# Performance work log

Measured on AMD Instinct MI355X. Metric: run time of the kernel, lower is better.

## Reference

```python
import jax, jax.numpy as jnp
import numpy as np

K = 20          # neighbors per point
EPS = 1e-5      # BatchNorm eps
SLOPE = 0.2     # LeakyReLU negative slope


def _knn(x, k):
    # x: [B, C, N] -> idx [B, N, k] of nearest neighbors in feature space
    sq = jnp.sum(x * x, axis=1)                       # [B, N]
    inner = jnp.einsum('bcn,bcm->bnm', x, x)          # [B, N, N]
    neg_dist = 2.0 * inner - sq[:, :, None] - sq[:, None, :]
    _, idx = jax.lax.top_k(neg_dist, k)
    return idx


def _edge_features(x, idx):
    # x: [B, C, N], idx: [B, N, k] -> edge features [B, 2C, N, k] = cat(x_i, x_j - x_i)
    xt = jnp.transpose(x, (0, 2, 1))                  # [B, N, C]
    nb = jax.vmap(lambda f, i: f[i])(xt, idx)         # [B, N, k, C]
    center = jnp.broadcast_to(xt[:, :, None, :], nb.shape)
    ef = jnp.concatenate([center, nb - center], axis=-1)  # [B, N, k, 2C]
    return jnp.transpose(ef, (0, 3, 1, 2))            # [B, 2C, N, k]


def _bn(t, g, b, axes):
    # BatchNorm (training-mode batch stats), channel axis = 1
    m = jnp.mean(t, axis=axes, keepdims=True)
    v = jnp.var(t, axis=axes, keepdims=True)
    tn = (t - m) * jax.lax.rsqrt(v + EPS)
    shp = [1] * t.ndim
    shp[1] = -1
    return tn * g.reshape(shp) + b.reshape(shp)


def _lrelu(t):
    return jnp.where(t >= 0, t, SLOPE * t)


def _layer2d(t, w, g, b):
    # 1x1 Conv2d (no bias) + BN2d + LeakyReLU over edge tensor [B, C, N, k]
    t = jnp.einsum('bcnk,oc->bonk', t, w)
    return _lrelu(_bn(t, g, b, (0, 2, 3)))


def _multi_edge_conv(x, w1, g1, b1, w2, g2, b2):
    idx = _knn(x, K)
    t = _edge_features(x, idx)
    t = _layer2d(t, w1, g1, b1)
    t = _layer2d(t, w2, g2, b2)
    return jnp.max(t, axis=-1)                        # max over neighbors -> [B, O, N]


def _edge_conv(x, w, g, b):
    idx = _knn(x, K)
    t = _edge_features(x, idx)
    t = _layer2d(t, w, g, b)
    return jnp.max(t, axis=-1)


def _tail(x, w, g, b):
    # 1x1 Conv1d (no bias) + BN1d + LeakyReLU, x: [B, 256, N] -> [B, 128, N]
    t = jnp.einsum('bcn,oc->bon', x, w)
    return _lrelu(_bn(t, g, b, (0, 2)))


def setup_inputs() -> dict:
    key = jax.random.key(0)
    ks = jax.random.split(key, 16)
    B, C, N = 8, 6, 2048

    def w(k, o, i):
        return jax.random.normal(k, (o, i), jnp.float32) * np.sqrt(2.0 / i).astype(np.float32)

    d = {
        'x': jax.random.normal(ks[0], (B, C, N), jnp.float32),
        # MultiEdgeConvolution 0: edge dim 2*6=12 -> 64 -> 64
        'w0a': w(ks[1], 64, 12), 'g0a': jnp.ones(64), 'b0a': jnp.zeros(64),
        'w0b': w(ks[2], 64, 64), 'g0b': jnp.ones(64), 'b0b': jnp.zeros(64),
        # MultiEdgeConvolution 1: edge dim 2*64=128 -> 64 -> 64
        'w1a': w(ks[3], 64, 128), 'g1a': jnp.ones(64), 'b1a': jnp.zeros(64),
        'w1b': w(ks[4], 64, 64), 'g1b': jnp.ones(64), 'b1b': jnp.zeros(64),
        # EdgeConvolution 2 and 3: 128 -> 64
        'w2': w(ks[5], 64, 128), 'g2': jnp.ones(64), 'b2': jnp.zeros(64),
        'w3': w(ks[6], 64, 128), 'g3': jnp.ones(64), 'b3': jnp.zeros(64),
        # Tail: 256 -> 128
        'wt': w(ks[7], 128, 256), 'gt': jnp.ones(128), 'bt': jnp.zeros(128),
    }
    return d


def reference(x, w0a, g0a, b0a, w0b, g0b, b0b,
              w1a, g1a, b1a, w1b, g1b, b1b,
              w2, g2, b2, w3, g3, b3, wt, gt, bt):
    x1 = _multi_edge_conv(x,  w0a, g0a, b0a, w0b, g0b, b0b)   # [B, 64, N]
    x2 = _multi_edge_conv(x1, w1a, g1a, b1a, w1b, g1b, b1b)   # [B, 64, N]
    x3 = _edge_conv(x2, w2, g2, b2)                           # [B, 64, N]
    x4 = _edge_conv(x3, w3, g3, b3)                           # [B, 64, N]
    feats = jnp.concatenate([x1, x2, x3, x4], axis=1)         # [B, 256, N]
    return _tail(feats, wt, gt, bt)                           # [B, 128, N]
```

## Files before the change

### kernel.cpp

```cpp
#include <hip/hip_runtime.h>

constexpr int BB = 8, NN = 2048, KK = 20;
constexpr float SLP = 0.2f;
constexpr float NEG = -3.0e38f;
constexpr float EMPTYV = -3.3e38f;
constexpr double EPSD = 1e-5;

typedef short short8 __attribute__((ext_vector_type(8)));
typedef float f32x4 __attribute__((ext_vector_type(4)));
typedef unsigned short ushort;

__device__ __forceinline__ float lrelu(float v) { return v >= 0.f ? v : SLP * v; }

__device__ __forceinline__ float bits2f(unsigned u) { union { unsigned u; float f; } a; a.u = u; return a.f; }
__device__ __forceinline__ unsigned f2bits(float f) { union { float f; unsigned u; } a; a.f = f; return a.u; }

__device__ __forceinline__ ushort bf16rne(float f) {
  unsigned u = f2bits(f);
  return (ushort)((u + 0x7fffu + ((u >> 16) & 1u)) >> 16);
}

__device__ __forceinline__ void split3(float x, ushort& h, ushort& m, ushort& l) {
  h = bf16rne(x);
  float fh = bits2f(((unsigned)h) << 16);
  float t1 = x - fh;
  m = bf16rne(t1);
  float fm = bits2f(((unsigned)m) << 16);
  float t2 = t1 - fm;
  l = bf16rne(t2);
}

__global__ __launch_bounds__(256) void k_prep0(const float* __restrict__ x, float* __restrict__ x0nc,
                                               ushort* __restrict__ xh, ushort* __restrict__ xm,
                                               ushort* __restrict__ xlo, float* __restrict__ sqb) {
  int i = blockIdx.x * 256 + threadIdx.x;
  if (i >= BB * NN) return;
  int b = i >> 11, n = i & (NN - 1);
  float v[6];
#pragma unroll
  for (int c = 0; c < 6; ++c) v[c] = x[((size_t)b * 6 + c) * NN + n];
  float s = 0.f;
#pragma unroll
  for (int c = 0; c < 6; ++c) s = __fadd_rn(s, __fmul_rn(v[c], v[c]));
  sqb[i] = s;
#pragma unroll
  for (int c = 0; c < 6; ++c) x0nc[(size_t)i * 6 + c] = v[c];
  size_t base = (size_t)i * 32;
#pragma unroll
  for (int c = 0; c < 32; ++c) {
    float xv = (c < 6) ? v[c] : 0.f;
    ushort h, m, l;
    split3(xv, h, m, l);
    xh[base + c] = h; xm[base + c] = m; xlo[base + c] = l;
  }
}

__global__ __launch_bounds__(256) void k_applyprep(float* __restrict__ xio, const double* __restrict__ st,
                                                   const float* __restrict__ g, const float* __restrict__ bb,
                                                   ushort* __restrict__ xh, ushort* __restrict__ xm,
                                                   ushort* __restrict__ xlo, float* __restrict__ sqb) {
  __shared__ float sa[64], sd[64];
  const int tid = threadIdx.x;
  if (tid < 64) {
    constexpr double invM = 1.0 / (double)(BB * NN * KK);
    double sm = st[tid] * invM;
    double ad = (double)g[tid] / sqrt(st[64 + tid] * invM - sm * sm + EPSD);
    sa[tid] = (float)ad;
    sd[tid] = (float)((double)bb[tid] - sm * ad);
  }
  __syncthreads();
  int i = blockIdx.x * 256 + tid;
  float* src = xio + (size_t)i * 64;
  float v[64];
#pragma unroll
  for (int c4 = 0; c4 < 16; ++c4) {
    float4 t = *reinterpret_cast<const float4*>(src + 4 * c4);
    v[4 * c4 + 0] = t.x; v[4 * c4 + 1] = t.y; v[4 * c4 + 2] = t.z; v[4 * c4 + 3] = t.w;
  }
#pragma unroll
  for (int c = 0; c < 64; ++c) v[c] = lrelu(fmaf(sa[c], v[c], sd[c]));
  float s = 0.f;
#pragma unroll
  for (int c = 0; c < 64; ++c) s = __fadd_rn(s, __fmul_rn(v[c], v[c]));
  sqb[i] = s;
#pragma unroll
  for (int c4 = 0; c4 < 16; ++c4) {
    float4 t;
    t.x = v[4 * c4 + 0]; t.y = v[4 * c4 + 1]; t.z = v[4 * c4 + 2]; t.w = v[4 * c4 + 3];
    *reinterpret_cast<float4*>(src + 4 * c4) = t;
  }
  size_t base = (size_t)i * 64;
#pragma unroll
  for (int c = 0; c < 64; ++c) {
    ushort h, m, l;
    split3(v[c], h, m, l);
    xh[base + c] = h; xm[base + c] = m; xlo[base + c] = l;
  }
}

template <int CP>
__global__ __launch_bounds__(256) void k_gram(const ushort* __restrict__ xh, const ushort* __restrict__ xm,
                                              const ushort* __restrict__ xlo, const float* __restrict__ sqb,
                                              float* __restrict__ S, int b0) {
  constexpr int KS = CP / 32;
  const int bl = blockIdx.z, b = b0 + bl;
  const int r0 = blockIdx.x * 32;
  const int cc0 = blockIdx.y * 32;
  const int tid = threadIdx.x, w = tid >> 6, l = tid & 63;
  const int rt = w & 1;
  const size_t xb = (size_t)b * NN * CP;
  const int ko = (l >> 4) * 8;

  short8 Ah[KS], Am[KS], Al[KS];
  const int ar = r0 + rt * 16 + (l & 15);
#pragma unroll
  for (int ks = 0; ks < KS; ++ks) {
    size_t o = xb + (size_t)ar * CP + ks * 32 + ko;
    Ah[ks] = *reinterpret_cast<const short8*>(xh + o);
    Am[ks] = *reinterpret_cast<const short8*>(xm + o);
    Al[ks] = *reinterpret_cast<const short8*>(xlo + o);
  }
  float sqi[4];
  const int rr = r0 + rt * 16 + (l >> 4) * 4;
#pragma unroll
  for (int q = 0; q < 4; ++q) sqi[q] = sqb[b * NN + rr + q];
  const size_t Sbase = ((size_t)bl * NN + rr) * NN;

  int ct = cc0 + (w >> 1);
  short8 Bh[KS], Bm[KS], Bl[KS], Ch[KS], Cm[KS], Cl[KS];
#pragma unroll
  for (int ks = 0; ks < KS; ++ks) {
    size_t o = xb + (size_t)(ct * 16 + (l & 15)) * CP + ks * 32 + ko;
    Bh[ks] = *reinterpret_cast<const short8*>(xh + o);
    Bm[ks] = *reinterpret_cast<const short8*>(xm + o);
    Bl[ks] = *reinterpret_cast<const short8*>(xlo + o);
  }
  for (int t = 0; t < 16; ++t) {
    int nct = ct + 2;
    if (t < 15) {
#pragma unroll
      for (int ks = 0; ks < KS; ++ks) {
        size_t o = xb + (size_t)(nct * 16 + (l & 15)) * CP + ks * 32 + ko;
        Ch[ks] = *reinterpret_cast<const short8*>(xh + o);
        Cm[ks] = *reinterpret_cast<const short8*>(xm + o);
        Cl[ks] = *reinterpret_cast<const short8*>(xlo + o);
      }
    }
    f32x4 acc = {0.f, 0.f, 0.f, 0.f};
#pragma unroll
    for (int ks = 0; ks < KS; ++ks) {
      acc = __builtin_amdgcn_mfma_f32_16x16x32_bf16(Am[ks], Bm[ks], acc, 0, 0, 0);
      acc = __builtin_amdgcn_mfma_f32_16x16x32_bf16(Ah[ks], Bl[ks], acc, 0, 0, 0);
      acc = __builtin_amdgcn_mfma_f32_16x16x32_bf16(Al[ks], Bh[ks], acc, 0, 0, 0);
      acc = __builtin_amdgcn_mfma_f32_16x16x32_bf16(Ah[ks], Bm[ks], acc, 0, 0, 0);
      acc = __builtin_amdgcn_mfma_f32_16x16x32_bf16(Am[ks], Bh[ks], acc, 0, 0, 0);
      acc = __builtin_amdgcn_mfma_f32_16x16x32_bf16(Ah[ks], Bh[ks], acc, 0, 0, 0);
    }
    int col = ct * 16 + (l & 15);
    float sqj = sqb[b * NN + col];
#pragma unroll
    for (int q = 0; q < 4; ++q) {
      float sc = __fsub_rn(__fsub_rn(2.f * acc[q], sqi[q]), sqj);
      S[Sbase + (size_t)q * NN + col] = sc;
    }
#pragma unroll
    for (int ks = 0; ks < KS; ++ks) { Bh[ks] = Ch[ks]; Bm[ks] = Cm[ks]; Bl[ks] = Cl[ks]; }
    ct = nct;
  }
}

__global__ __launch_bounds__(256) void k_select(const float* __restrict__ S, int* __restrict__ idxo, int b0) {
  const int bl = blockIdx.y, b = b0 + bl;
  const int wv = threadIdx.x >> 6, l = threadIdx.x & 63;
  const int row = blockIdx.x * 4 + wv;
  __shared__ float sr[4][2048];
  __shared__ int oid[4][20];
  char* base = reinterpret_cast<char*>(&sr[wv][0]);
  const float* Sp = S + ((size_t)bl * NN + row) * NN;
#pragma unroll
  for (int e = 0; e < 8; ++e) {
    float4 v = *reinterpret_cast<const float4*>(Sp + e * 256 + l * 4);
    int c = e * 64 + l;
    c ^= (c >> 3) & 7;
    *reinterpret_cast<float4*>(base + (c << 4)) = v;
  }
  float v0 = EMPTYV, v1 = EMPTYV;
  int i0 = -1, i1 = -1;
#pragma unroll
  for (int e = 0; e < 8; ++e) {
    int c = l * 8 + e;
    c ^= (c >> 3) & 7;
    float4 v = *reinterpret_cast<const float4*>(base + (c << 4));
    int jb = l * 32 + e * 4;
    float va[4] = {v.x, v.y, v.z, v.w};
#pragma unroll
    for (int q = 0; q < 4; ++q) {
      float vv = va[q];
      int jj = jb + q;
      if (vv > v0) { v1 = v0; i1 = i0; v0 = vv; i0 = jj; }
      else if (vv > v1) { v1 = vv; i1 = jj; }
    }
  }
  for (int e = 0; e < KK; ++e) {
    float m = v0;
#pragma unroll
    for (int d = 1; d < 64; d <<= 1) m = fmaxf(m, __shfl_xor(m, d));
    unsigned long long msk = __ballot(v0 == m);
    int wl = __ffsll((unsigned long long)msk) - 1;
    if (l == wl) {
      oid[wv][e] = i0;
      int j = i0;
      int cc = j >> 2;
      int cs = cc ^ ((cc >> 3) & 7);
      *reinterpret_cast<float*>(base + (cs << 4) + ((j & 3) << 2)) = NEG;
      v0 = v1; i0 = i1; v1 = EMPTYV; i1 = -1;
      if (v0 <= EMPTYV) {
        v0 = EMPTYV; v1 = EMPTYV; i0 = -1; i1 = -1;
#pragma unroll
        for (int e2 = 0; e2 < 8; ++e2) {
          int c = l * 8 + e2;
          c ^= (c >> 3) & 7;
          float4 v = *reinterpret_cast<const float4*>(base + (c << 4));
          int jb = l * 32 + e2 * 4;
          float va[4] = {v.x, v.y, v.z, v.w};
#pragma unroll
          for (int q = 0; q < 4; ++q) {
            float vv = va[q];
            int jj = jb + q;
            if (vv > v0) { v1 = v0; i1 = i0; v0 = vv; i0 = jj; }
            else if (vv > v1) { v1 = vv; i1 = jj; }
          }
        }
      }
    }
  }
  if (l < KK) idxo[((size_t)b * NN + row) * KK + l] = oid[wv][l];
}

template <int C>
__global__ __launch_bounds__(256) void k_uv(const float* __restrict__ xin, const float* __restrict__ w,
                                            float* __restrict__ u, float* __restrict__ v) {
  const int b = blockIdx.y, n0 = blockIdx.x * 4;
  const int tid = threadIdx.x, o = tid & 63, nn = tid >> 6;
  __shared__ float wl[64][2 * C + 1];
  __shared__ float xl[4][C];
  for (int t = tid; t < 64 * 2 * C; t += 256) wl[t / (2 * C)][t % (2 * C)] = w[t];
  for (int t = tid; t < 4 * C; t += 256) xl[t / C][t % C] = xin[((size_t)b * NN + n0 + t / C) * C + t % C];
  __syncthreads();
  float s1 = 0.f, s2 = 0.f;
#pragma unroll
  for (int c = 0; c < C; ++c) {
    float xv = xl[nn][c];
    s1 = fmaf(wl[o][c], xv, s1);
    s2 = fmaf(wl[o][C + c], xv, s2);
  }
  size_t i = ((size_t)b * NN + n0 + nn) * 64 + o;
  u[i] = s1 - s2;
  v[i] = s2;
}

__global__ __launch_bounds__(256) void k_passA(const float* __restrict__ u, const float* __restrict__ v,
                                               const int* __restrict__ idx, double* __restrict__ st) {
  const int b = blockIdx.y, n0 = blockIdx.x * 16;
  const int tid = threadIdx.x, c = tid & 63, nw = tid >> 6;
  double s = 0.0, ss = 0.0;
  for (int nn = nw; nn < 16; nn += 4) {
    size_t nb = (size_t)b * NN + n0 + nn;
    float uu = u[nb * 64 + c];
    const int* ip = idx + nb * KK;
#pragma unroll
    for (int k = 0; k < KK; ++k) {
      float val = uu + v[((size_t)b * NN + ip[k]) * 64 + c];
      double dv = (double)val;
      s += dv; ss = fma(dv, dv, ss);
    }
  }
  __shared__ double red[2][4][64];
  red[0][nw][c] = s; red[1][nw][c] = ss;
  __syncthreads();
  if (tid < 64) {
    double S = red[0][0][tid] + red[0][1][tid] + red[0][2][tid] + red[0][3][tid];
    double SS = red[1][0][tid] + red[1][1][tid] + red[1][2][tid] + red[1][3][tid];
    atomicAdd(&st[tid], S);
    atomicAdd(&st[64 + tid], SS);
  }
}

__global__ __launch_bounds__(256) void k_passAmax(const float* __restrict__ u, const float* __restrict__ v,
                                                  const int* __restrict__ idx, float* __restrict__ xout,
                                                  double* __restrict__ st) {
  const int b = blockIdx.y, n0 = blockIdx.x * 16;
  const int tid = threadIdx.x, c = tid & 63, nw = tid >> 6;
  double s = 0.0, ss = 0.0;
  for (int nn = nw; nn < 16; nn += 4) {
    size_t nb = (size_t)b * NN + n0 + nn;
    float uu = u[nb * 64 + c];
    const int* ip = idx + nb * KK;
    float mx = NEG;
#pragma unroll
    for (int k = 0; k < KK; ++k) {
      float val = uu + v[((size_t)b * NN + ip[k]) * 64 + c];
      mx = fmaxf(mx, val);
      double dv = (double)val;
      s += dv; ss = fma(dv, dv, ss);
    }
    xout[nb * 64 + c] = mx;
  }
  __shared__ double red[2][4][64];
  red[0][nw][c] = s; red[1][nw][c] = ss;
  __syncthreads();
  if (tid < 64) {
    double S = red[0][0][tid] + red[0][1][tid] + red[0][2][tid] + red[0][3][tid];
    double SS = red[1][0][tid] + red[1][1][tid] + red[1][2][tid] + red[1][3][tid];
    atomicAdd(&st[tid], S);
    atomicAdd(&st[64 + tid], SS);
  }
}

__global__ __launch_bounds__(256) void k_passB(const float* __restrict__ u, const float* __restrict__ v,
                                               const int* __restrict__ idx, const double* __restrict__ st1,
                                               const float* __restrict__ g1, const float* __restrict__ b1,
                                               const float* __restrict__ w2, float* __restrict__ xout,
                                               double* __restrict__ st2) {
  const int b = blockIdx.y, n0 = blockIdx.x * 8;
  const int tid = threadIdx.x, lane = tid & 63, wv = tid >> 6;
  __shared__ __align__(16) float buf[160][68];
  constexpr double invM = 1.0 / (double)(BB * NN * KK);
  double sm = st1[lane] * invM;
  double ad = (double)g1[lane] / sqrt(st1[64 + lane] * invM - sm * sm + EPSD);
  float a = (float)ad;
  float d = (float)((double)b1[lane] - sm * ad);

  for (int p = wv; p < 160; p += 4) {
    int nn = p / 20, k = p - nn * 20;
    size_t nb = (size_t)b * NN + n0 + nn;
    int j = idx[nb * KK + k];
    float val = u[nb * 64 + lane] + v[((size_t)b * NN + j) * 64 + lane];
    buf[p][lane] = lrelu(fmaf(a, val, d));
  }
  __syncthreads();

  const int row = wv * 64 + lane;
  const bool active = row < 160;
  float ar[64];
  if (active) {
#pragma unroll
    for (int c4 = 0; c4 < 16; ++c4) {
      float4 t4 = *reinterpret_cast<const float4*>(&buf[row][4 * c4]);
      ar[4 * c4 + 0] = t4.x; ar[4 * c4 + 1] = t4.y;
      ar[4 * c4 + 2] = t4.z; ar[4 * c4 + 3] = t4.w;
    }
  }
  __syncthreads();

#pragma unroll 2
  for (int o = 0; o < 64; ++o) {
    if (active) {
      const float* wp = w2 + o * 64;
      float a0 = 0.f, a1 = 0.f, a2 = 0.f, a3 = 0.f;
#pragma unroll
      for (int c4 = 0; c4 < 16; ++c4) {
        float4 w4 = *reinterpret_cast<const float4*>(wp + 4 * c4);
        a0 = fmaf(w4.x, ar[4 * c4 + 0], a0);
        a1 = fmaf(w4.y, ar[4 * c4 + 1], a1);
        a2 = fmaf(w4.z, ar[4 * c4 + 2], a2);
        a3 = fmaf(w4.w, ar[4 * c4 + 3], a3);
      }
      buf[row][o] = (a0 + a1) + (a2 + a3);
    }
  }
  __syncthreads();

  double s2 = 0.0, ss2 = 0.0;
#pragma unroll
  for (int q = 0; q < 2; ++q) {
    int nl = 2 * wv + q;
    float mx = NEG;
#pragma unroll 4
    for (int k = 0; k < KK; ++k) {
      float t2v = buf[nl * 20 + k][lane];
      mx = fmaxf(mx, t2v);
      double dv = (double)t2v;
      s2 += dv; ss2 = fma(dv, dv, ss2);
    }
    xout[((size_t)b * NN + n0 + nl) * 64 + lane] = mx;
  }
  __syncthreads();
  double* red = reinterpret_cast<double*>(&buf[0][0]);
  red[wv * 64 + lane] = s2;
  red[256 + wv * 64 + lane] = ss2;
  __syncthreads();
  if (tid < 64) {
    double S = red[tid] + red[64 + tid] + red[128 + tid] + red[192 + tid];
    double SS = red[256 + tid] + red[320 + tid] + red[384 + tid] + red[448 + tid];
    atomicAdd(&st2[tid], S);
    atomicAdd(&st2[64 + tid], SS);
  }
}

__global__ __launch_bounds__(256) void k_apply(float* __restrict__ xio, const double* __restrict__ st,
                                               const float* __restrict__ g, const float* __restrict__ bb,
                                               double invM) {
  const int b = blockIdx.y, n0 = blockIdx.x * 4;
  const int tid = threadIdx.x, c = tid & 63, nn = tid >> 6;
  double sm = st[c] * invM;
  double ad = (double)g[c] / sqrt(st[64 + c] * invM - sm * sm + EPSD);
  float a = (float)ad;
  float d = (float)((double)bb[c] - sm * ad);
  size_t i = ((size_t)b * NN + n0 + nn) * 64 + c;
  xio[i] = lrelu(fmaf(a, xio[i], d));
}

__global__ __launch_bounds__(256) void k_wtT(const float* __restrict__ wt, float* __restrict__ wtT) {
  int i = blockIdx.x * 256 + threadIdx.x;
  if (i < 128 * 256) { int o = i >> 8, c = i & 255; wtT[c * 128 + o] = wt[i]; }
}

__global__ __launch_bounds__(256) void k_tail(const float* __restrict__ x1, const float* __restrict__ x2,
                                              const float* __restrict__ x3, const float* __restrict__ x4,
                                              const float* __restrict__ wtT, float* __restrict__ tt) {
  const int b = blockIdx.y, n0 = blockIdx.x * 16;
  const int tid = threadIdx.x, og = tid & 31, nt = tid >> 5;
  __shared__ float xc[256][20];
  const float* xs[4] = {x1, x2, x3, x4};
  for (int t = tid; t < 4096; t += 256) {
    int n = t >> 8, c = t & 255;
    xc[c][n] = xs[c >> 6][((size_t)b * NN + n0 + n) * 64 + (c & 63)];
  }
  __syncthreads();
  float acc[4][2];
#pragma unroll
  for (int r = 0; r < 4; ++r) { acc[r][0] = 0.f; acc[r][1] = 0.f; }
#pragma unroll 4
  for (int c = 0; c < 256; ++c) {
    float4 wv = *reinterpret_cast<const float4*>(&wtT[(size_t)c * 128 + 4 * og]);
    float xc0 = xc[c][2 * nt], xc1 = xc[c][2 * nt + 1];
    acc[0][0] = fmaf(wv.x, xc0, acc[0][0]); acc[0][1] = fmaf(wv.x, xc1, acc[0][1]);
    acc[1][0] = fmaf(wv.y, xc0, acc[1][0]); acc[1][1] = fmaf(wv.y, xc1, acc[1][1]);
    acc[2][0] = fmaf(wv.z, xc0, acc[2][0]); acc[2][1] = fmaf(wv.z, xc1, acc[2][1]);
    acc[3][0] = fmaf(wv.w, xc0, acc[3][0]); acc[3][1] = fmaf(wv.w, xc1, acc[3][1]);
  }
#pragma unroll
  for (int q = 0; q < 2; ++q) {
    float4 o4;
    o4.x = acc[0][q]; o4.y = acc[1][q]; o4.z = acc[2][q]; o4.w = acc[3][q];
    *reinterpret_cast<float4*>(&tt[((size_t)b * NN + n0 + 2 * nt + q) * 128 + 4 * og]) = o4;
  }
}

__global__ __launch_bounds__(256) void k_tailstats(const float* __restrict__ tt, double* __restrict__ st) {
  const int tid = threadIdx.x, c = tid & 127, h = tid >> 7;
  const int r0 = blockIdx.x * 32;
  double s = 0.0, ss = 0.0;
  for (int rr = h; rr < 32; rr += 2) {
    double val = (double)tt[(size_t)(r0 + rr) * 128 + c];
    s += val; ss = fma(val, val, ss);
  }
  __shared__ double red[2][2][128];
  red[0][h][c] = s; red[1][h][c] = ss;
  __syncthreads();
  if (tid < 128) {
    atomicAdd(&st[tid], red[0][0][tid] + red[0][1][tid]);
    atomicAdd(&st[128 + tid], red[1][0][tid] + red[1][1][tid]);
  }
}

__global__ __launch_bounds__(256) void k_tailapply(const float* __restrict__ tt, const double* __restrict__ st,
                                                   const float* __restrict__ g, const float* __restrict__ bb,
                                                   float* __restrict__ out) {
  const int b = blockIdx.y, n0 = blockIdx.x * 64;
  const int tid = threadIdx.x;
  __shared__ float tl[128][65];
  constexpr double invM = 1.0 / (double)(BB * NN);
  {
    const int o = tid & 127, h = tid >> 7;
    double sm = st[o] * invM;
    double ad = (double)g[o] / sqrt(st[128 + o] * invM - sm * sm + EPSD);
    float a = (float)ad;
    float d = (float)((double)bb[o] - sm * ad);
    for (int nn2 = h; nn2 < 64; nn2 += 2) {
      float val = tt[((size_t)b * NN + n0 + nn2) * 128 + o];
      tl[o][nn2] = lrelu(fmaf(a, val, d));
    }
  }
  __syncthreads();
  {
    const int nl = tid & 63, ow = tid >> 6;
    for (int o = ow; o < 128; o += 4)
      out[((size_t)b * 128 + o) * NN + n0 + nl] = tl[o][nl];
  }
}

extern "C" void kernel_launch(void* const* d_in, const int* in_sizes, int n_in,
                              void* d_out, int out_size, void* d_ws, size_t ws_size,
                              hipStream_t stream) {
  const float* x = (const float*)d_in[0];
  const float* w0a = (const float*)d_in[1];
  const float* g0a = (const float*)d_in[2];
  const float* b0a = (const float*)d_in[3];
  const float* w0b = (const float*)d_in[4];
  const float* g0b = (const float*)d_in[5];
  const float* b0b = (const float*)d_in[6];
  const float* w1a = (const float*)d_in[7];
  const float* g1a = (const float*)d_in[8];
  const float* b1a = (const float*)d_in[9];
  const float* w1b = (const float*)d_in[10];
  const float* g1b = (const float*)d_in[11];
  const float* b1b = (const float*)d_in[12];
  const float* w2 = (const float*)d_in[13];
  const float* g2 = (const float*)d_in[14];
  const float* b2 = (const float*)d_in[15];
  const float* w3 = (const float*)d_in[16];
  const float* g3 = (const float*)d_in[17];
  const float* b3 = (const float*)d_in[18];
  const float* wt = (const float*)d_in[19];
  const float* gt = (const float*)d_in[20];
  const float* bt = (const float*)d_in[21];
  float* out = (float*)d_out;

  char* p = (char*)d_ws;
  double* stA = (double*)p; p += 2048;
  double* stB = (double*)p; p += 2048;
  double* stT = (double*)p; p += 2048;
  ushort* xh = (ushort*)p; p += (size_t)BB * NN * 64 * 2;
  ushort* xm = (ushort*)p; p += (size_t)BB * NN * 64 * 2;
  ushort* xlo = (ushort*)p; p += (size_t)BB * NN * 64 * 2;
  float* sqb = (float*)p; p += (size_t)BB * NN * 4;
  float* x0nc = (float*)p; p += (size_t)BB * NN * 6 * 4;
  float* x1 = (float*)p; p += (size_t)BB * NN * 64 * 4;
  float* x2 = (float*)p; p += (size_t)BB * NN * 64 * 4;
  float* x3 = (float*)p; p += (size_t)BB * NN * 64 * 4;
  float* x4 = (float*)p; p += (size_t)BB * NN * 64 * 4;
  float* ub = (float*)p; p += (size_t)BB * NN * 64 * 4;
  float* vb = (float*)p; p += (size_t)BB * NN * 64 * 4;
  float* ttl = (float*)p; p += (size_t)BB * NN * 128 * 4;
  float* wtTb = (float*)p; p += 128 * 256 * 4;
  int* idx = (int*)p; p += (size_t)BB * NN * KK * 4;
  size_t base_bytes = (size_t)(p - (char*)d_ws);
  const size_t SBYTES = (size_t)NN * NN * 4;

  float* S;
  int bc;
  if (ws_size >= base_bytes + SBYTES) {
    S = (float*)(((uintptr_t)p + 255) & ~(uintptr_t)255);
    size_t avail = ws_size - ((char*)S - (char*)d_ws);
    bc = (int)(avail / SBYTES);
    if (bc > BB) bc = BB;
    if (bc < 1) { S = ub; bc = 1; }
  } else {
    S = ub;
    bc = 1;
  }

  constexpr double invMe = 1.0 / (double)(BB * NN * KK);
  dim3 blk(256);

  auto knn = [&](int stage) {
    for (int c = 0; c < BB; c += bc) {
      int nb = BB - c < bc ? BB - c : bc;
      if (stage == 0)
        k_gram<32><<<dim3(NN / 32, 4, nb), blk, 0, stream>>>(xh, xm, xlo, sqb, S, c);
      else
        k_gram<64><<<dim3(NN / 32, 4, nb), blk, 0, stream>>>(xh, xm, xlo, sqb, S, c);
      k_select<<<dim3(NN / 4, nb), blk, 0, stream>>>(S, idx, c);
    }
  };

  k_prep0<<<dim3(BB * NN / 256), blk, 0, stream>>>(x, x0nc, xh, xm, xlo, sqb);
  knn(0);
  k_uv<6><<<dim3(NN / 4, BB), blk, 0, stream>>>(x0nc, w0a, ub, vb);
  hipMemsetAsync(stA, 0, 2048, stream);
  k_passA<<<dim3(NN / 16, BB), blk, 0, stream>>>(ub, vb, idx, stA);
  hipMemsetAsync(stB, 0, 2048, stream);
  k_passB<<<dim3(NN / 8, BB), blk, 0, stream>>>(ub, vb, idx, stA, g0a, b0a, w0b, x1, stB);
  k_applyprep<<<dim3(BB * NN / 256), blk, 0, stream>>>(x1, stB, g0b, b0b, xh, xm, xlo, sqb);

  knn(1);
  k_uv<64><<<dim3(NN / 4, BB), blk, 0, stream>>>(x1, w1a, ub, vb);
  hipMemsetAsync(stA, 0, 2048, stream);
  k_passA<<<dim3(NN / 16, BB), blk, 0, stream>>>(ub, vb, idx, stA);
  hipMemsetAsync(stB, 0, 2048, stream);
  k_passB<<<dim3(NN / 8, BB), blk, 0, stream>>>(ub, vb, idx, stA, g1a, b1a, w1b, x2, stB);
  k_applyprep<<<dim3(BB * NN / 256), blk, 0, stream>>>(x2, stB, g1b, b1b, xh, xm, xlo, sqb);

  knn(2);
  k_uv<64><<<dim3(NN / 4, BB), blk, 0, stream>>>(x2, w2, ub, vb);
  hipMemsetAsync(stA, 0, 2048, stream);
  k_passAmax<<<dim3(NN / 16, BB), blk, 0, stream>>>(ub, vb, idx, x3, stA);
  k_applyprep<<<dim3(BB * NN / 256), blk, 0, stream>>>(x3, stA, g2, b2, xh, xm, xlo, sqb);

  knn(3);
  k_uv<64><<<dim3(NN / 4, BB), blk, 0, stream>>>(x3, w3, ub, vb);
  hipMemsetAsync(stA, 0, 2048, stream);
  k_passAmax<<<dim3(NN / 16, BB), blk, 0, stream>>>(ub, vb, idx, x4, stA);
  k_apply<<<dim3(NN / 4, BB), blk, 0, stream>>>(x4, stA, g3, b3, invMe);

  k_wtT<<<dim3(128), blk, 0, stream>>>(wt, wtTb);
  k_tail<<<dim3(NN / 16, BB), blk, 0, stream>>>(x1, x2, x3, x4, wtTb, ttl);
  hipMemsetAsync(stT, 0, 2048, stream);
  k_tailstats<<<dim3(512), blk, 0, stream>>>(ttl, stT);
  k_tailapply<<<dim3(NN / 64, BB), blk, 0, stream>>>(ttl, stT, gt, bt, out);
}
```

Before: 1.139 ms.

## Fuse Gram matrix and top-k selection into one kNN kernel, restructure passB conv

Replaces the separate Gram-matrix kernel, which wrote a full NxN score matrix to global memory, and the row-wise selection kernel with a single fused kernel. It computes 16 rows' scores in 512-column chunks in shared memory and maintains a running top-20 list using packed 64-bit value/index keys and wavefront reductions. This removes the large global round-trip of the score matrix and the batch-chunked launch loop, at the cost of more complex per-chunk merge logic and lower parallelism per block. It also changes passB to hold the second conv's weights in registers and compute the conv inside the max/stat loop, and merges two stat memsets into one.

New measurement: 1.686 ms. 1.48x slower.

```diff
diff --git a/kernel.cpp b/kernel.cpp
--- a/kernel.cpp
+++ b/kernel.cpp
@@ -3,12 +3,12 @@
 constexpr int BB = 8, NN = 2048, KK = 20;
 constexpr float SLP = 0.2f;
 constexpr float NEG = -3.0e38f;
-constexpr float EMPTYV = -3.3e38f;
 constexpr double EPSD = 1e-5;
 
 typedef short short8 __attribute__((ext_vector_type(8)));
 typedef float f32x4 __attribute__((ext_vector_type(4)));
 typedef unsigned short ushort;
+typedef unsigned long long u64;
 
 __device__ __forceinline__ float lrelu(float v) { return v >= 0.f ? v : SLP * v; }
 
@@ -28,6 +28,26 @@
   float fm = bits2f(((unsigned)m) << 16);
   float t2 = t1 - fm;
   l = bf16rne(t2);
+}
+
+__device__ __forceinline__ u64 mkkey(float v, int j) {
+  unsigned u = f2bits(v);
+  unsigned k32 = (u >> 31) ? ~u : (u | 0x80000000u);
+  return ((u64)k32 << 32) | (unsigned)(~(unsigned)j);
+}
+__device__ __forceinline__ float keyval(u64 k) {
+  unsigned k32 = (unsigned)(k >> 32);
+  unsigned u = (k32 & 0x80000000u) ? (k32 ^ 0x80000000u) : ~k32;
+  return bits2f(u);
+}
+__device__ __forceinline__ int keyidx(u64 k) { return (int)(~(unsigned)k); }
+__device__ __forceinline__ u64 wavemax64(u64 k) {
+#pragma unroll
+  for (int d = 1; d < 64; d <<= 1) {
+    u64 o = __shfl_xor(k, d);
+    if (o > k) k = o;
+  }
+  return k;
 }
 
 __global__ __launch_bounds__(256) void k_prep0(const float* __restrict__ x, float* __restrict__ x0nc,
@@ -99,142 +119,145 @@
 }
 
 template <int CP>
-__global__ __launch_bounds__(256) void k_gram(const ushort* __restrict__ xh, const ushort* __restrict__ xm,
+__global__ __launch_bounds__(256) void k_knnf(const ushort* __restrict__ xh, const ushort* __restrict__ xm,
                                               const ushort* __restrict__ xlo, const float* __restrict__ sqb,
-                                              float* __restrict__ S, int b0) {
+                                              int* __restrict__ idxo) {
   constexpr int KS = CP / 32;
-  const int bl = blockIdx.z, b = b0 + bl;
-  const int r0 = blockIdx.x * 32;
-  const int cc0 = blockIdx.y * 32;
+  const int flat = blockIdx.x + gridDim.x * blockIdx.y;
+  const int b = flat & 7;
+  const int r0 = (flat >> 3) * 16;
   const int tid = threadIdx.x, w = tid >> 6, l = tid & 63;
-  const int rt = w & 1;
   const size_t xb = (size_t)b * NN * CP;
   const int ko = (l >> 4) * 8;
 
+  __shared__ __align__(16) float sc[16 * 513];
+  __shared__ float lv[16][20];
+  __shared__ int li[16][20];
+
   short8 Ah[KS], Am[KS], Al[KS];
-  const int ar = r0 + rt * 16 + (l & 15);
-#pragma unroll
-  for (int ks = 0; ks < KS; ++ks) {
-    size_t o = xb + (size_t)ar * CP + ks * 32 + ko;
-    Ah[ks] = *reinterpret_cast<const short8*>(xh + o);
-    Am[ks] = *reinterpret_cast<const short8*>(xm + o);
-    Al[ks] = *reinterpret_cast<const short8*>(xlo + o);
+  {
+    const int ar = r0 + (l & 15);
+#pragma unroll
+    for (int ks = 0; ks < KS; ++ks) {
+      size_t o = xb + (size_t)ar * CP + ks * 32 + ko;
+      Ah[ks] = *reinterpret_cast<const short8*>(xh + o);
+      Am[ks] = *reinterpret_cast<const short8*>(xm + o);
+      Al[ks] = *reinterpret_cast<const short8*>(xlo + o);
+    }
   }
   float sqi[4];
-  const int rr = r0 + rt * 16 + (l >> 4) * 4;
-#pragma unroll
-  for (int q = 0; q < 4; ++q) sqi[q] = sqb[b * NN + rr + q];
-  const size_t Sbase = ((size_t)bl * NN + rr) * NN;
-
-  int ct = cc0 + (w >> 1);
-  short8 Bh[KS], Bm[KS], Bl[KS], Ch[KS], Cm[KS], Cl[KS];
-#pragma unroll
-  for (int ks = 0; ks < KS; ++ks) {
-    size_t o = xb + (size_t)(ct * 16 + (l & 15)) * CP + ks * 32 + ko;
-    Bh[ks] = *reinterpret_cast<const short8*>(xh + o);
-    Bm[ks] = *reinterpret_cast<const short8*>(xm + o);
-    Bl[ks] = *reinterpret_cast<const short8*>(xlo + o);
-  }
-  for (int t = 0; t < 16; ++t) {
-    int nct = ct + 2;
-    if (t < 15) {
+#pragma unroll
+  for (int q = 0; q < 4; ++q) sqi[q] = sqb[b * NN + r0 + (l >> 4) * 4 + q];
+  const int myrow0 = w * 4;
+
+  for (int chunk = 0; chunk < 4; ++chunk) {
+    int ct = chunk * 32 + w * 8;
+    short8 Bh[KS], Bm[KS], Bl[KS], Ch[KS], Cm[KS], Cl[KS];
+#pragma unroll
+    for (int ks = 0; ks < KS; ++ks) {
+      size_t o = xb + (size_t)(ct * 16 + (l & 15)) * CP + ks * 32 + ko;
+      Bh[ks] = *reinterpret_cast<const short8*>(xh + o);
+      Bm[ks] = *reinterpret_cast<const short8*>(xm + o);
+      Bl[ks] = *reinterpret_cast<const short8*>(xlo + o);
+    }
+    for (int t8 = 0; t8 < 8; ++t8) {
+      if (t8 < 7) {
+#pragma unroll
+        for (int ks = 0; ks < KS; ++ks) {
+          size_t o = xb + (size_t)((ct + 1) * 16 + (l & 15)) * CP + ks * 32 + ko;
+          Ch[ks] = *reinterpret_cast<const short8*>(xh + o);
+          Cm[ks] = *reinterpret_cast<const short8*>(xm + o);
+          Cl[ks] = *reinterpret_cast<const short8*>(xlo + o);
+        }
+      }
+      f32x4 acc = {0.f, 0.f, 0.f, 0.f};
 #pragma unroll
       for (int ks = 0; ks < KS; ++ks) {
-        size_t o = xb + (size_t)(nct * 16 + (l & 15)) * CP + ks * 32 + ko;
-        Ch[ks] = *reinterpret_cast<const short8*>(xh + o);
-        Cm[ks] = *reinterpret_cast<const short8*>(xm + o);
-        Cl[ks] = *reinterpret_cast<const short8*>(xlo + o);
+        acc = __builtin_amdgcn_mfma_f32_16x16x32_bf16(Am[ks], Bm[ks], acc, 0, 0, 0);
+        acc = __builtin_amdgcn_mfma_f32_16x16x32_bf16(Ah[ks], Bl[ks], acc, 0, 0, 0);
+        acc = __builtin_amdgcn_mfma_f32_16x16x32_bf16(Al[ks], Bh[ks], acc, 0, 0, 0);
+        acc = __builtin_amdgcn_mfma_f32_16x16x32_bf16(Ah[ks], Bm[ks], acc, 0, 0, 0);
+        acc = __builtin_amdgcn_mfma_f32_16x16x32_bf16(Am[ks], Bh[ks], acc, 0, 0, 0);
+        acc = __builtin_amdgcn_mfma_f32_16x16x32_bf16(Ah[ks], Bh[ks], acc, 0, 0, 0);
       }
-    }
-    f32x4 acc = {0.f, 0.f, 0.f, 0.f};
-#pragma unroll
-    for (int ks = 0; ks < KS; ++ks) {
-      acc = __builtin_amdgcn_mfma_f32_16x16x32_bf16(Am[ks], Bm[ks], acc, 0, 0, 0);
-      acc = __builtin_amdgcn_mfma_f32_16x16x32_bf16(Ah[ks], Bl[ks], acc, 0, 0, 0);
-      acc = __builtin_amdgcn_mfma_f32_16x16x32_bf16(Al[ks], Bh[ks], acc, 0, 0, 0);
-      acc = __builtin_amdgcn_mfma_f32_16x16x32_bf16(Ah[ks], Bm[ks], acc, 0, 0, 0);
-      acc = __builtin_amdgcn_mfma_f32_16x16x32_bf16(Am[ks], Bh[ks], acc, 0, 0, 0);
-      acc = __builtin_amdgcn_mfma_f32_16x16x32_bf16(Ah[ks], Bh[ks], acc, 0, 0, 0);
-    }
-    int col = ct * 16 + (l & 15);
-    float sqj = sqb[b * NN + col];
-#pragma unroll
-    for (int q = 0; q < 4; ++q) {
-      float sc = __fsub_rn(__fsub_rn(2.f * acc[q], sqi[q]), sqj);
-      S[Sbase + (size_t)q * NN + col] = sc;
-    }
-#pragma unroll
-    for (int ks = 0; ks < KS; ++ks) { Bh[ks] = Ch[ks]; Bm[ks] = Cm[ks]; Bl[ks] = Cl[ks]; }
-    ct = nct;
-  }
-}
-
-__global__ __launch_bounds__(256) void k_select(const float* __restrict__ S, int* __restrict__ idxo, int b0) {
-  const int bl = blockIdx.y, b = b0 + bl;
-  const int wv = threadIdx.x >> 6, l = threadIdx.x & 63;
-  const int row = blockIdx.x * 4 + wv;
-  __shared__ float sr[4][2048];
-  __shared__ int oid[4][20];
-  char* base = reinterpret_cast<char*>(&sr[wv][0]);
-  const float* Sp = S + ((size_t)bl * NN + row) * NN;
-#pragma unroll
-  for (int e = 0; e < 8; ++e) {
-    float4 v = *reinterpret_cast<const float4*>(Sp + e * 256 + l * 4);
-    int c = e * 64 + l;
-    c ^= (c >> 3) & 7;
-    *reinterpret_cast<float4*>(base + (c << 4)) = v;
-  }
-  float v0 = EMPTYV, v1 = EMPTYV;
-  int i0 = -1, i1 = -1;
-#pragma unroll
-  for (int e = 0; e < 8; ++e) {
-    int c = l * 8 + e;
-    c ^= (c >> 3) & 7;
-    float4 v = *reinterpret_cast<const float4*>(base + (c << 4));
-    int jb = l * 32 + e * 4;
-    float va[4] = {v.x, v.y, v.z, v.w};
-#pragma unroll
-    for (int q = 0; q < 4; ++q) {
-      float vv = va[q];
-      int jj = jb + q;
-      if (vv > v0) { v1 = v0; i1 = i0; v0 = vv; i0 = jj; }
-      else if (vv > v1) { v1 = vv; i1 = jj; }
-    }
-  }
-  for (int e = 0; e < KK; ++e) {
-    float m = v0;
-#pragma unroll
-    for (int d = 1; d < 64; d <<= 1) m = fmaxf(m, __shfl_xor(m, d));
-    unsigned long long msk = __ballot(v0 == m);
-    int wl = __ffsll((unsigned long long)msk) - 1;
-    if (l == wl) {
-      oid[wv][e] = i0;
-      int j = i0;
-      int cc = j >> 2;
-      int cs = cc ^ ((cc >> 3) & 7);
-      *reinterpret_cast<float*>(base + (cs << 4) + ((j & 3) << 2)) = NEG;
-      v0 = v1; i0 = i1; v1 = EMPTYV; i1 = -1;
-      if (v0 <= EMPTYV) {
-        v0 = EMPTYV; v1 = EMPTYV; i0 = -1; i1 = -1;
-#pragma unroll
-        for (int e2 = 0; e2 < 8; ++e2) {
-          int c = l * 8 + e2;
-          c ^= (c >> 3) & 7;
-          float4 v = *reinterpret_cast<const float4*>(base + (c << 4));
-          int jb = l * 32 + e2 * 4;
-          float va[4] = {v.x, v.y, v.z, v.w};
-#pragma unroll
-          for (int q = 0; q < 4; ++q) {
-            float vv = va[q];
-            int jj = jb + q;
-            if (vv > v0) { v1 = v0; i1 = i0; v0 = vv; i0 = jj; }
-            else if (vv > v1) { v1 = vv; i1 = jj; }
+      int col = ct * 16 + (l & 15);
+      float sqj = sqb[b * NN + col];
+      int cl = col - chunk * 512;
+#pragma unroll
+      for (int q = 0; q < 4; ++q) {
+        float s = __fsub_rn(__fsub_rn(2.f * acc[q], sqi[q]), sqj);
+        sc[((l >> 4) * 4 + q) * 513 + cl] = s;
+      }
+#pragma unroll
+      for (int ks = 0; ks < KS; ++ks) { Bh[ks] = Ch[ks]; Bm[ks] = Cm[ks]; Bl[ks] = Cl[ks]; }
+      ++ct;
+    }
+    __syncthreads();
+    for (int rr = 0; rr < 4; ++rr) {
+      const int row = myrow0 + rr;
+      u64 k[8];
+      float vmax = NEG;
+#pragma unroll
+      for (int m = 0; m < 8; ++m) {
+        float v = sc[row * 513 + l + 64 * m];
+        vmax = fmaxf(vmax, v);
+        k[m] = mkkey(v, chunk * 512 + l + 64 * m);
+      }
+      if (chunk == 0) {
+        u64 k0 = 0;
+#pragma unroll
+        for (int m = 0; m < 8; ++m) k0 = k[m] > k0 ? k[m] : k0;
+        for (int e = 0; e < KK; ++e) {
+          u64 wk = wavemax64(k0);
+          if (k0 == wk) {
+            lv[row][e] = keyval(wk);
+            li[row][e] = keyidx(wk);
+            u64 nk = 0;
+#pragma unroll
+            for (int m = 0; m < 8; ++m) {
+              if (k[m] == wk) k[m] = 0;
+              nk = k[m] > nk ? k[m] : nk;
+            }
+            k0 = nk;
+          }
+        }
+      } else {
+#pragma unroll
+        for (int d = 1; d < 64; d <<= 1) vmax = fmaxf(vmax, __shfl_xor(vmax, d));
+        if (vmax > lv[row][19]) {
+          while (true) {
+            float thr = lv[row][19];
+            u64 kthr = mkkey(thr, 0);
+            u64 k0 = 0;
+#pragma unroll
+            for (int m = 0; m < 8; ++m) k0 = k[m] > k0 ? k[m] : k0;
+            if (k0 <= kthr) k0 = 0;
+            u64 wk = wavemax64(k0);
+            if (wk == 0) break;
+            float nv = keyval(wk);
+            int nj = keyidx(wk);
+            float mylv = 0.f; int myli_ = 0;
+            u64 lk = 0;
+            if (l < 20) { mylv = lv[row][l]; myli_ = li[row][l]; lk = mkkey(mylv, myli_); }
+            int pos = __popcll(__ballot(lk > wk));
+            if (l >= pos && l < 19) { lv[row][l + 1] = mylv; li[row][l + 1] = myli_; }
+            if (l == pos) { lv[row][l] = nv; li[row][l] = nj; }
+            if (k0 == wk) {
+#pragma unroll
+              for (int m = 0; m < 8; ++m)
+                if (k[m] == wk) k[m] = 0;
+            }
           }
         }
       }
     }
-  }
-  if (l < KK) idxo[((size_t)b * NN + row) * KK + l] = oid[wv][l];
+    __syncthreads();
+  }
+#pragma unroll
+  for (int rr = 0; rr < 4; ++rr) {
+    int row = myrow0 + rr;
+    if (l < KK) idxo[((size_t)b * NN + r0 + row) * KK + l] = li[row][l];
+  }
 }
 
 template <int C>
@@ -324,53 +347,26 @@
                                                double* __restrict__ st2) {
   const int b = blockIdx.y, n0 = blockIdx.x * 8;
   const int tid = threadIdx.x, lane = tid & 63, wv = tid >> 6;
-  __shared__ __align__(16) float buf[160][68];
+  __shared__ __align__(16) float act[160][64];
   constexpr double invM = 1.0 / (double)(BB * NN * KK);
   double sm = st1[lane] * invM;
   double ad = (double)g1[lane] / sqrt(st1[64 + lane] * invM - sm * sm + EPSD);
   float a = (float)ad;
   float d = (float)((double)b1[lane] - sm * ad);
-
+  float wr[64];
+#pragma unroll
+  for (int c4 = 0; c4 < 16; ++c4) {
+    float4 t4 = *reinterpret_cast<const float4*>(w2 + (size_t)lane * 64 + 4 * c4);
+    wr[4 * c4 + 0] = t4.x; wr[4 * c4 + 1] = t4.y; wr[4 * c4 + 2] = t4.z; wr[4 * c4 + 3] = t4.w;
+  }
   for (int p = wv; p < 160; p += 4) {
     int nn = p / 20, k = p - nn * 20;
     size_t nb = (size_t)b * NN + n0 + nn;
     int j = idx[nb * KK + k];
     float val = u[nb * 64 + lane] + v[((size_t)b * NN + j) * 64 + lane];
-    buf[p][lane] = lrelu(fmaf(a, val, d));
-  }
-  __syncthreads();
-
-  const int row = wv * 64 + lane;
-  const bool active = row < 160;
-  float ar[64];
-  if (active) {
-#pragma unroll
-    for (int c4 = 0; c4 < 16; ++c4) {
-      float4 t4 = *reinterpret_cast<const float4*>(&buf[row][4 * c4]);
-      ar[4 * c4 + 0] = t4.x; ar[4 * c4 + 1] = t4.y;
-      ar[4 * c4 + 2] = t4.z; ar[4 * c4 + 3] = t4.w;
-    }
-  }
-  __syncthreads();
-
-#pragma unroll 2
-  for (int o = 0; o < 64; ++o) {
-    if (active) {
-      const float* wp = w2 + o * 64;
-      float a0 = 0.f, a1 = 0.f, a2 = 0.f, a3 = 0.f;
-#pragma unroll
-      for (int c4 = 0; c4 < 16; ++c4) {
-        float4 w4 = *reinterpret_cast<const float4*>(wp + 4 * c4);
-        a0 = fmaf(w4.x, ar[4 * c4 + 0], a0);
-        a1 = fmaf(w4.y, ar[4 * c4 + 1], a1);
-        a2 = fmaf(w4.z, ar[4 * c4 + 2], a2);
-        a3 = fmaf(w4.w, ar[4 * c4 + 3], a3);
-      }
-      buf[row][o] = (a0 + a1) + (a2 + a3);
-    }
-  }
-  __syncthreads();
-
+    act[p][lane] = lrelu(fmaf(a, val, d));
+  }
+  __syncthreads();
   double s2 = 0.0, ss2 = 0.0;
 #pragma unroll
   for (int q = 0; q < 2; ++q) {
@@ -378,7 +374,17 @@
     float mx = NEG;
 #pragma unroll 4
     for (int k = 0; k < KK; ++k) {
-      float t2v = buf[nl * 20 + k][lane];
+      const float* ap = &act[nl * 20 + k][0];
+      float a0 = 0.f, a1 = 0.f, a2 = 0.f, a3 = 0.f;
+#pragma unroll
+      for (int c4 = 0; c4 < 16; ++c4) {
+        float4 v4 = *reinterpret_cast<const float4*>(ap + 4 * c4);
+        a0 = fmaf(wr[4 * c4 + 0], v4.x, a0);
+        a1 = fmaf(wr[4 * c4 + 1], v4.y, a1);
+        a2 = fmaf(wr[4 * c4 + 2], v4.z, a2);
+        a3 = fmaf(wr[4 * c4 + 3], v4.w, a3);
+      }
+      float t2v = (a0 + a1) + (a2 + a3);
       mx = fmaxf(mx, t2v);
       double dv = (double)t2v;
       s2 += dv; ss2 = fma(dv, dv, ss2);
@@ -386,7 +392,7 @@
     xout[((size_t)b * NN + n0 + nl) * 64 + lane] = mx;
   }
   __syncthreads();
-  double* red = reinterpret_cast<double*>(&buf[0][0]);
+  double* red = reinterpret_cast<double*>(&act[0][0]);
   red[wv * 64 + lane] = s2;
   red[256 + wv * 64 + lane] = ss2;
   __syncthreads();
@@ -536,60 +542,33 @@
   float* ttl = (float*)p; p += (size_t)BB * NN * 128 * 4;
   float* wtTb = (float*)p; p += 128 * 256 * 4;
   int* idx = (int*)p; p += (size_t)BB * NN * KK * 4;
-  size_t base_bytes = (size_t)(p - (char*)d_ws);
-  const size_t SBYTES = (size_t)NN * NN * 4;
-
-  float* S;
-  int bc;
-  if (ws_size >= base_bytes + SBYTES) {
-    S = (float*)(((uintptr_t)p + 255) & ~(uintptr_t)255);
-    size_t avail = ws_size - ((char*)S - (char*)d_ws);
-    bc = (int)(avail / SBYTES);
-    if (bc > BB) bc = BB;
-    if (bc < 1) { S = ub; bc = 1; }
-  } else {
-    S = ub;
-    bc = 1;
-  }
 
   constexpr double invMe = 1.0 / (double)(BB * NN * KK);
   dim3 blk(256);
-
-  auto knn = [&](int stage) {
-    for (int c = 0; c < BB; c += bc) {
-      int nb = BB - c < bc ? BB - c : bc;
-      if (stage == 0)
-        k_gram<32><<<dim3(NN / 32, 4, nb), blk, 0, stream>>>(xh, xm, xlo, sqb, S, c);
-      else
-        k_gram<64><<<dim3(NN / 32, 4, nb), blk, 0, stream>>>(xh, xm, xlo, sqb, S, c);
-      k_select<<<dim3(NN / 4, nb), blk, 0, stream>>>(S, idx, c);
-    }
-  };
+  dim3 kgrid(NN / 16, BB);
 
   k_prep0<<<dim3(BB * NN / 256), blk, 0, stream>>>(x, x0nc, xh, xm, xlo, sqb);
-  knn(0);
+  k_knnf<32><<<kgrid, blk, 0, stream>>>(xh, xm, xlo, sqb, idx);
   k_uv<6><<<dim3(NN / 4, BB), blk, 0, stream>>>(x0nc, w0a, ub, vb);
-  hipMemsetAsync(stA, 0, 2048, stream);
+  hipMemsetAsync(stA, 0, 4096, stream);
   k_passA<<<dim3(NN / 16, BB), blk, 0, stream>>>(ub, vb, idx, stA);
-  hipMemsetAsync(stB, 0, 2048, stream);
   k_passB<<<dim3(NN / 8, BB), blk, 0, stream>>>(ub, vb, idx, stA, g0a, b0a, w0b, x1, stB);
   k_applyprep<<<dim3(BB * NN / 256), blk, 0, stream>>>(x1, stB, g0b, b0b, xh, xm, xlo, sqb);
 
-  knn(1);
+  k_knnf<64><<<kgrid, blk, 0, stream>>>(xh, xm, xlo, sqb, idx);
   k_uv<64><<<dim3(NN / 4, BB), blk, 0, stream>>>(x1, w1a, ub, vb);
-  hipMemsetAsync(stA, 0, 2048, stream);
+  hipMemsetAsync(stA, 0, 4096, stream);
   k_passA<<<dim3(NN / 16, BB), blk, 0, stream>>>(ub, vb, idx, stA);
-  hipMemsetAsync(stB, 0, 2048, stream);
   k_passB<<<dim3(NN / 8, BB), blk, 0, stream>>>(ub, vb, idx, stA, g1a, b1a, w1b, x2, stB);
   k_applyprep<<<dim3(BB * NN / 256), blk, 0, stream>>>(x2, stB, g1b, b1b, xh, xm, xlo, sqb);
 
-  knn(2);
+  k_knnf<64><<<kgrid, blk, 0, stream>>>(xh, xm, xlo, sqb, idx);
   k_uv<64><<<dim3(NN / 4, BB), blk, 0, stream>>>(x2, w2, ub, vb);
   hipMemsetAsync(stA, 0, 2048, stream);
   k_passAmax<<<dim3(NN / 16, BB), blk, 0, stream>>>(ub, vb, idx, x3, stA);
   k_applyprep<<<dim3(BB * NN / 256), blk, 0, stream>>>(x3, stA, g2, b2, xh, xm, xlo, sqb);
 
-  knn(3);
+  k_knnf<64><<<kgrid, blk, 0, stream>>>(xh, xm, xlo, sqb, idx);
   k_uv<64><<<dim3(NN / 4, BB), blk, 0, stream>>>(x3, w3, ub, vb);
   hipMemsetAsync(stA, 0, 2048, stream);
   k_passAmax<<<dim3(NN / 16, BB), blk, 0, stream>>>(ub, vb, idx, x4, stA);
```

## Keep conv2 weights in registers per output channel and merge stat memsets

Applied to the files above, without the earlier changes.

Restructures k_passB so each lane owns one output channel, holds that channel's 64 weights in registers, and computes the second 1x1 conv on the fly inside the max/stat loop. Activations are read from LDS as broadcast float4 loads. This drops the intermediate LDS write-back pass, two barriers, and the repeated global weight loads per output. It also replaces two memsets with a single 4096-byte memset, which assumes stB directly follows stA in memory. The cost is 64 extra registers per thread, and only 2 of the 8 rows per wave do work, so compute parallelism per block falls.

Measured after the change: 1.067 ms. 1.07x faster.

```diff
diff --git a/kernel.cpp b/kernel.cpp
--- a/kernel.cpp
+++ b/kernel.cpp
@@ -324,53 +324,26 @@
                                                double* __restrict__ st2) {
   const int b = blockIdx.y, n0 = blockIdx.x * 8;
   const int tid = threadIdx.x, lane = tid & 63, wv = tid >> 6;
-  __shared__ __align__(16) float buf[160][68];
+  __shared__ __align__(16) float act[160][64];
   constexpr double invM = 1.0 / (double)(BB * NN * KK);
   double sm = st1[lane] * invM;
   double ad = (double)g1[lane] / sqrt(st1[64 + lane] * invM - sm * sm + EPSD);
   float a = (float)ad;
   float d = (float)((double)b1[lane] - sm * ad);
-
+  float wr[64];
+#pragma unroll
+  for (int c4 = 0; c4 < 16; ++c4) {
+    float4 t4 = *reinterpret_cast<const float4*>(w2 + (size_t)lane * 64 + 4 * c4);
+    wr[4 * c4 + 0] = t4.x; wr[4 * c4 + 1] = t4.y; wr[4 * c4 + 2] = t4.z; wr[4 * c4 + 3] = t4.w;
+  }
   for (int p = wv; p < 160; p += 4) {
     int nn = p / 20, k = p - nn * 20;
     size_t nb = (size_t)b * NN + n0 + nn;
     int j = idx[nb * KK + k];
     float val = u[nb * 64 + lane] + v[((size_t)b * NN + j) * 64 + lane];
-    buf[p][lane] = lrelu(fmaf(a, val, d));
-  }
-  __syncthreads();
-
-  const int row = wv * 64 + lane;
-  const bool active = row < 160;
-  float ar[64];
-  if (active) {
-#pragma unroll
-    for (int c4 = 0; c4 < 16; ++c4) {
-      float4 t4 = *reinterpret_cast<const float4*>(&buf[row][4 * c4]);
-      ar[4 * c4 + 0] = t4.x; ar[4 * c4 + 1] = t4.y;
-      ar[4 * c4 + 2] = t4.z; ar[4 * c4 + 3] = t4.w;
-    }
-  }
-  __syncthreads();
-
-#pragma unroll 2
-  for (int o = 0; o < 64; ++o) {
-    if (active) {
-      const float* wp = w2 + o * 64;
-      float a0 = 0.f, a1 = 0.f, a2 = 0.f, a3 = 0.f;
-#pragma unroll
-      for (int c4 = 0; c4 < 16; ++c4) {
-        float4 w4 = *reinterpret_cast<const float4*>(wp + 4 * c4);
-        a0 = fmaf(w4.x, ar[4 * c4 + 0], a0);
-        a1 = fmaf(w4.y, ar[4 * c4 + 1], a1);
-        a2 = fmaf(w4.z, ar[4 * c4 + 2], a2);
-        a3 = fmaf(w4.w, ar[4 * c4 + 3], a3);
-      }
-      buf[row][o] = (a0 + a1) + (a2 + a3);
-    }
-  }
-  __syncthreads();
-
+    act[p][lane] = lrelu(fmaf(a, val, d));
+  }
+  __syncthreads();
   double s2 = 0.0, ss2 = 0.0;
 #pragma unroll
   for (int q = 0; q < 2; ++q) {
@@ -378,7 +351,17 @@
     float mx = NEG;
 #pragma unroll 4
     for (int k = 0; k < KK; ++k) {
-      float t2v = buf[nl * 20 + k][lane];
+      const float* ap = &act[nl * 20 + k][0];
+      float a0 = 0.f, a1 = 0.f, a2 = 0.f, a3 = 0.f;
+#pragma unroll
+      for (int c4 = 0; c4 < 16; ++c4) {
+        float4 v4 = *reinterpret_cast<const float4*>(ap + 4 * c4);
+        a0 = fmaf(wr[4 * c4 + 0], v4.x, a0);
+        a1 = fmaf(wr[4 * c4 + 1], v4.y, a1);
+        a2 = fmaf(wr[4 * c4 + 2], v4.z, a2);
+        a3 = fmaf(wr[4 * c4 + 3], v4.w, a3);
+      }
+      float t2v = (a0 + a1) + (a2 + a3);
       mx = fmaxf(mx, t2v);
       double dv = (double)t2v;
       s2 += dv; ss2 = fma(dv, dv, ss2);
@@ -386,7 +369,7 @@
     xout[((size_t)b * NN + n0 + nl) * 64 + lane] = mx;
   }
   __syncthreads();
-  double* red = reinterpret_cast<double*>(&buf[0][0]);
+  double* red = reinterpret_cast<double*>(&act[0][0]);
   red[wv * 64 + lane] = s2;
   red[256 + wv * 64 + lane] = ss2;
   __syncthreads();
@@ -569,17 +552,15 @@
   k_prep0<<<dim3(BB * NN / 256), blk, 0, stream>>>(x, x0nc, xh, xm, xlo, sqb);
   knn(0);
   k_uv<6><<<dim3(NN / 4, BB), blk, 0, stream>>>(x0nc, w0a, ub, vb);
-  hipMemsetAsync(stA, 0, 2048, stream);
+  hipMemsetAsync(stA, 0, 4096, stream);
   k_passA<<<dim3(NN / 16, BB), blk, 0, stream>>>(ub, vb, idx, stA);
-  hipMemsetAsync(stB, 0, 2048, stream);
   k_passB<<<dim3(NN / 8, BB), blk, 0, stream>>>(ub, vb, idx, stA, g0a, b0a, w0b, x1, stB);
   k_applyprep<<<dim3(BB * NN / 256), blk, 0, stream>>>(x1, stB, g0b, b0b, xh, xm, xlo, sqb);
 
   knn(1);
   k_uv<64><<<dim3(NN / 4, BB), blk, 0, stream>>>(x1, w1a, ub, vb);
-  hipMemsetAsync(stA, 0, 2048, stream);
+  hipMemsetAsync(stA, 0, 4096, stream);
   k_passA<<<dim3(NN / 16, BB), blk, 0, stream>>>(ub, vb, idx, stA);
-  hipMemsetAsync(stB, 0, 2048, stream);
   k_passB<<<dim3(NN / 8, BB), blk, 0, stream>>>(ub, vb, idx, stA, g1a, b1a, w1b, x2, stB);
   k_applyprep<<<dim3(BB * NN / 256), blk, 0, stream>>>(x2, stB, g1b, b1b, xh, xm, xlo, sqb);
 
```
